# Kernel tuning notes

Hardware: AMD Instinct MI355X
Metric: run time of the kernel (lower is better)

Reference implementation:

```python
import jax, jax.numpy as jnp
import numpy as np

B, N, S, HEADS, D = 8, 512, 64, 16, 256

def setup_inputs() -> dict:
    key = jax.random.key(0)
    ks = jax.random.split(key, 5)
    spatial_pos = jax.random.randint(ks[0], (B, N, S), 0, N)
    H = jax.random.normal(ks[1], (B, N, D), dtype=jnp.float32)
    A = jax.random.uniform(ks[2], (B, N, N), dtype=jnp.float32)
    sigma = jnp.ones((1,), dtype=jnp.float32)
    spatial_emb = jax.random.normal(ks[3], (N, HEADS), dtype=jnp.float32)
    vt_weight = jax.random.normal(ks[4], (1, HEADS), dtype=jnp.float32)
    return {"spatial_pos": spatial_pos, "H": H, "A": A, "sigma": sigma,
            "spatial_emb": spatial_emb, "vt_weight": vt_weight}

def reference(spatial_pos, H, A, sigma, spatial_emb, vt_weight):
    b, n, s = spatial_pos.shape
    heads = spatial_emb.shape[1]
    # padding_idx=0: row 0 of the embedding table is zero
    emb = spatial_emb.at[0].set(0.0)
    spb = emb[spatial_pos]                       # [B, N, S, heads]
    # torch .view reinterprets contiguous memory: reshape, NOT transpose
    spb = spb.reshape(b, heads, n, s)            # [B, heads, N, S]
    spatial_bias = jnp.einsum('bhns,bhms->bhnm', spb, spb)  # [B,heads,N,N]
    # degree-normalized (left) adjacency aggregation
    deg = jnp.sum(A, axis=-1, keepdims=True)     # [B, N, 1]
    nor_A = (deg ** -0.5) * A
    M = jnp.matmul(nor_A, H)                     # [B, N, D]
    # pairwise squared euclidean distance via expansion (same math,
    # avoids materializing [B,N,N,D])
    h2 = jnp.sum(H * H, axis=-1)                 # [B, N]
    m2 = jnp.sum(M * M, axis=-1)                 # [B, N]
    cross = jnp.einsum('bnd,bmd->bnm', H, M)     # [B, N, N]
    d2 = h2[:, :, None] + m2[:, None, :] - 2.0 * cross
    gaussian = jnp.exp(-d2 / (2.0 * sigma[0] ** 2))  # [B, N, N]
    # virtual-token bias (vt_weight) only touches padded row/col 0,
    # which is sliced off before return -> no effect on output.
    return spatial_bias + gaussian[:, None, :, :]  # [B, heads, N, N]
```

## Files before the change

kernel.cpp:

```cpp
#include <hip/hip_runtime.h>
#include <hip/hip_bf16.h>

#define NB 8
#define NN 512
#define NS 64
#define NH 16
#define ND 256

typedef __attribute__((ext_vector_type(8))) short bf16x8;
typedef __attribute__((ext_vector_type(4))) short bf16x4;
typedef __attribute__((ext_vector_type(4))) float f32x4;

__device__ inline float wred(float v) {
#pragma unroll
  for (int m = 32; m; m >>= 1) v += __shfl_xor(v, m, 64);
  return v;
}
__device__ inline float wred16(float v) {
#pragma unroll
  for (int m = 1; m < 16; m <<= 1) v += __shfl_xor(v, m, 64);
  return v;
}
__device__ inline ushort f2bf(float x) {
  __hip_bfloat16 h = __float2bfloat16(x);
  return *(ushort*)&h;
}

__global__ __launch_bounds__(256) void k_prep(const int* __restrict__ pos,
                                              const float* __restrict__ emb,
                                              const float* __restrict__ H,
                                              const float* __restrict__ A,
                                              __hip_bfloat16* __restrict__ spb,
                                              __hip_bfloat16* __restrict__ Ab,
                                              __hip_bfloat16* __restrict__ Hb,
                                              __hip_bfloat16* __restrict__ HT,
                                              float* __restrict__ rdeg,
                                              float* __restrict__ h2) {
  __shared__ ushort T[64][68];
  int blk = blockIdx.x, tid = threadIdx.x;
  int wave = tid >> 6, lane = tid & 63;

  if (blk < 1024) {
    int t = blk * 256 + tid;
    int idx = pos[t];
    __hip_bfloat16* dst = spb + (size_t)t * NH;
    union { bf16x8 v; ushort h[8]; } u0, u1;
    if (idx == 0) {
#pragma unroll
      for (int i = 0; i < 8; ++i) { u0.h[i] = 0; u1.h[i] = 0; }
    } else {
      const float* er = emb + idx * NH;
#pragma unroll
      for (int i = 0; i < 8; ++i) { u0.h[i] = f2bf(er[i]); u1.h[i] = f2bf(er[8 + i]); }
    }
    *(bf16x8*)(void*)dst = u0.v;
    *(bf16x8*)(void*)(dst + 8) = u1.v;
  } else if (blk < 2048) {
    int row = (blk - 1024) * 4 + wave;
    const float* ar = A + (size_t)row * NN;
    float4 v0 = *(const float4*)(ar + lane * 8);
    float4 v1 = *(const float4*)(ar + lane * 8 + 4);
    float s = v0.x + v0.y + v0.z + v0.w + v1.x + v1.y + v1.z + v1.w;
    union { bf16x8 v; ushort h[8]; } u;
    u.h[0] = f2bf(v0.x); u.h[1] = f2bf(v0.y); u.h[2] = f2bf(v0.z); u.h[3] = f2bf(v0.w);
    u.h[4] = f2bf(v1.x); u.h[5] = f2bf(v1.y); u.h[6] = f2bf(v1.z); u.h[7] = f2bf(v1.w);
    *(bf16x8*)(void*)(Ab + (size_t)row * NN + lane * 8) = u.v;
    s = wred(s);
    if (lane == 0) rdeg[row] = rsqrtf(s);
  } else if (blk < 3072) {
    int row = (blk - 2048) * 4 + wave;
    const float* hr = H + (size_t)row * ND;
    float4 v = *(const float4*)(hr + lane * 4);
    float ss = v.x * v.x + v.y * v.y + v.z * v.z + v.w * v.w;
    union { bf16x4 v4; ushort h[4]; } u;
    u.h[0] = f2bf(v.x); u.h[1] = f2bf(v.y); u.h[2] = f2bf(v.z); u.h[3] = f2bf(v.w);
    *(bf16x4*)(void*)(Hb + (size_t)row * ND + lane * 4) = u.v4;
    ss = wred(ss);
    if (lane == 0) h2[row] = ss;
  } else {
    int bi = blk - 3072;
    int b = bi >> 5, r = bi & 31;
    int d0 = (r >> 3) * 64, n0 = (r & 7) * 64;
    int n = tid >> 2, c = (tid & 3) * 16;
    const float* src = H + ((size_t)b * NN + n0 + n) * ND + d0 + c;
#pragma unroll
    for (int q = 0; q < 4; ++q) {
      float4 f = *(const float4*)(src + q * 4);
      T[n][c + q * 4 + 0] = f2bf(f.x);
      T[n][c + q * 4 + 1] = f2bf(f.y);
      T[n][c + q * 4 + 2] = f2bf(f.z);
      T[n][c + q * 4 + 3] = f2bf(f.w);
    }
    __syncthreads();
    int d = tid >> 2, nc = (tid & 3) * 16;
    union { bf16x8 v; ushort h[8]; } o0, o1;
#pragma unroll
    for (int i = 0; i < 8; ++i) { o0.h[i] = T[nc + i][d]; o1.h[i] = T[nc + 8 + i][d]; }
    __hip_bfloat16* dst = HT + ((size_t)b * ND + d0 + d) * NN + n0 + nc;
    *(bf16x8*)(void*)dst = o0.v;
    *(bf16x8*)(void*)(dst + 8) = o1.v;
  }
}

__global__ __launch_bounds__(256) void k_gemmM(const __hip_bfloat16* __restrict__ Ab,
                                               const __hip_bfloat16* __restrict__ HT,
                                               const float* __restrict__ rdeg,
                                               __hip_bfloat16* __restrict__ Mb,
                                               float* __restrict__ m2p) {
  int wave = threadIdx.x >> 6, lane = threadIdx.x & 63;
  int b = blockIdx.x & 7, t = blockIdx.x >> 3;
  int tile = t * 4 + wave;
  int rt = tile >> 3, ct = tile & 7;
  int r0 = rt * 32, c0 = ct * 32;
  int rl = lane & 15, g4 = lane >> 4;
  const __hip_bfloat16* X = Ab + (size_t)b * NN * NN;
  const __hip_bfloat16* Y = HT + (size_t)b * ND * NN;
  f32x4 acc[2][2];
#pragma unroll
  for (int i = 0; i < 2; ++i)
#pragma unroll
    for (int j = 0; j < 2; ++j) { acc[i][j][0] = 0.f; acc[i][j][1] = 0.f; acc[i][j][2] = 0.f; acc[i][j][3] = 0.f; }
#pragma unroll
  for (int kk = 0; kk < NN / 32; ++kk) {
    int kb = kk * 32 + g4 * 8;
    bf16x8 a[2], bv[2];
#pragma unroll
    for (int i = 0; i < 2; ++i)
      a[i] = *(const bf16x8*)(const void*)(X + (size_t)(r0 + i * 16 + rl) * NN + kb);
#pragma unroll
    for (int j = 0; j < 2; ++j)
      bv[j] = *(const bf16x8*)(const void*)(Y + (size_t)(c0 + j * 16 + rl) * NN + kb);
#pragma unroll
    for (int i = 0; i < 2; ++i)
#pragma unroll
      for (int j = 0; j < 2; ++j)
        acc[i][j] = __builtin_amdgcn_mfma_f32_16x16x32_bf16(a[i], bv[j], acc[i][j], 0, 0, 0);
  }
#pragma unroll
  for (int i = 0; i < 2; ++i)
#pragma unroll
    for (int r = 0; r < 4; ++r) {
      int row = r0 + i * 16 + g4 * 4 + r;
      float rd = rdeg[b * NN + row];
      float ss = 0.f;
#pragma unroll
      for (int j = 0; j < 2; ++j) {
        float m = rd * acc[i][j][r];
        int col = c0 + j * 16 + rl;
        Mb[((size_t)b * NN + row) * ND + col] = __float2bfloat16(m);
        ss += m * m;
      }
      ss = wred16(ss);
      if (rl == 0) m2p[(size_t)ct * (NB * NN) + b * NN + row] = ss;
    }
}

__global__ __launch_bounds__(256) void k_out(const __hip_bfloat16* __restrict__ Hb,
                                             const __hip_bfloat16* __restrict__ Mb,
                                             const __hip_bfloat16* __restrict__ spb,
                                             const float* __restrict__ h2,
                                             const float* __restrict__ m2p,
                                             const float* __restrict__ sigma,
                                             float* __restrict__ out) {
  __shared__ float Gt[64][66];
  __shared__ float h2s[64], m2s[64];
  int b = blockIdx.x & 7;
  int t2 = blockIdx.x >> 3;
  int ct = t2 & 7, rt = (t2 >> 3) & 7, hg = t2 >> 6;
  int r0 = rt * 64, c0 = ct * 64;
  int tid = threadIdx.x;
  int wave = tid >> 6, lane = tid & 63;
  int rl = lane & 15, g4 = lane >> 4;

  if (tid < 64) {
    h2s[tid] = h2[b * NN + r0 + tid];
  } else if (tid < 128) {
    int c = tid - 64;
    float s = 0.f;
#pragma unroll
    for (int p = 0; p < 8; ++p) s += m2p[(size_t)p * (NB * NN) + b * NN + c0 + c];
    m2s[c] = s;
  }
  __syncthreads();

  {
    const __hip_bfloat16* X = Hb + (size_t)b * NN * ND;
    const __hip_bfloat16* Y = Mb + (size_t)b * NN * ND;
    int rbase = r0 + wave * 16;
    f32x4 acc[4];
#pragma unroll
    for (int j = 0; j < 4; ++j) { acc[j][0] = 0.f; acc[j][1] = 0.f; acc[j][2] = 0.f; acc[j][3] = 0.f; }
#pragma unroll
    for (int kk = 0; kk < ND / 32; ++kk) {
      int kb = kk * 32 + g4 * 8;
      bf16x8 a = *(const bf16x8*)(const void*)(X + (size_t)(rbase + rl) * ND + kb);
#pragma unroll
      for (int j = 0; j < 4; ++j) {
        bf16x8 bv = *(const bf16x8*)(const void*)(Y + (size_t)(c0 + j * 16 + rl) * ND + kb);
        acc[j] = __builtin_amdgcn_mfma_f32_16x16x32_bf16(a, bv, acc[j], 0, 0, 0);
      }
    }
    float sg = sigma[0];
    float inv = 0.5f / (sg * sg);
#pragma unroll
    for (int j = 0; j < 4; ++j)
#pragma unroll
      for (int r = 0; r < 4; ++r) {
        int rowl = wave * 16 + g4 * 4 + r;
        int col = j * 16 + rl;
        float d2 = h2s[rowl] + m2s[col] - 2.0f * acc[j][r];
        Gt[rowl][col] = __expf(-d2 * inv);
      }
  }
  __syncthreads();

#pragma unroll
  for (int hh = 0; hh < 2; ++hh) {
    int h = hg * 8 + wave * 2 + hh;
    const __hip_bfloat16* X = spb + ((size_t)b * NH + h) * NN * NS;
    f32x4 acc[4][4];
#pragma unroll
    for (int i = 0; i < 4; ++i)
#pragma unroll
      for (int j = 0; j < 4; ++j) { acc[i][j][0] = 0.f; acc[i][j][1] = 0.f; acc[i][j][2] = 0.f; acc[i][j][3] = 0.f; }
#pragma unroll
    for (int kk = 0; kk < NS / 32; ++kk) {
      int kb = kk * 32 + g4 * 8;
      bf16x8 a[4], bv[4];
#pragma unroll
      for (int i = 0; i < 4; ++i)
        a[i] = *(const bf16x8*)(const void*)(X + (size_t)(r0 + i * 16 + rl) * NS + kb);
#pragma unroll
      for (int j = 0; j < 4; ++j)
        bv[j] = *(const bf16x8*)(const void*)(X + (size_t)(c0 + j * 16 + rl) * NS + kb);
#pragma unroll
      for (int i = 0; i < 4; ++i)
#pragma unroll
        for (int j = 0; j < 4; ++j)
          acc[i][j] = __builtin_amdgcn_mfma_f32_16x16x32_bf16(a[i], bv[j], acc[i][j], 0, 0, 0);
    }
    float* ob = out + ((size_t)b * NH + h) * NN * NN;
#pragma unroll
    for (int i = 0; i < 4; ++i)
#pragma unroll
      for (int j = 0; j < 4; ++j)
#pragma unroll
        for (int r = 0; r < 4; ++r) {
          int rowl = i * 16 + g4 * 4 + r;
          int col = j * 16 + rl;
          ob[(size_t)(r0 + rowl) * NN + c0 + col] = acc[i][j][r] + Gt[rowl][col];
        }
  }
}

extern "C" void kernel_launch(void* const* d_in, const int* in_sizes, int n_in,
                              void* d_out, int out_size, void* d_ws, size_t ws_size,
                              hipStream_t stream) {
  const int* pos = (const int*)d_in[0];
  const float* H = (const float*)d_in[1];
  const float* A = (const float*)d_in[2];
  const float* sigma = (const float*)d_in[3];
  const float* emb = (const float*)d_in[4];
  float* out = (float*)d_out;

  char* ws = (char*)d_ws;
  size_t off = 0;
  auto alloc = [&](size_t bytes) -> void* {
    void* p = ws + off;
    off = (off + bytes + 255) & ~(size_t)255;
    return p;
  };
  __hip_bfloat16* spb = (__hip_bfloat16*)alloc((size_t)NB * NH * NN * NS * 2);
  __hip_bfloat16* Ab  = (__hip_bfloat16*)alloc((size_t)NB * NN * NN * 2);
  __hip_bfloat16* Hb  = (__hip_bfloat16*)alloc((size_t)NB * NN * ND * 2);
  __hip_bfloat16* HT  = (__hip_bfloat16*)alloc((size_t)NB * ND * NN * 2);
  __hip_bfloat16* Mb  = (__hip_bfloat16*)alloc((size_t)NB * NN * ND * 2);
  float* m2p  = (float*)alloc((size_t)8 * NB * NN * 4);
  float* rdeg = (float*)alloc((size_t)NB * NN * 4);
  float* h2   = (float*)alloc((size_t)NB * NN * 4);

  k_prep<<<3328, 256, 0, stream>>>(pos, emb, H, A, spb, Ab, Hb, HT, rdeg, h2);
  k_gemmM<<<256, 256, 0, stream>>>(Ab, HT, rdeg, Mb, m2p);
  k_out<<<1024, 256, 0, stream>>>(Hb, Mb, spb, h2, m2p, sigma, out);
}
```

Before: 76.05 us.

## Stage output tiles through LDS for float4 stores, loop all heads per block

```diff
diff --git a/kernel.cpp b/kernel.cpp
--- a/kernel.cpp
+++ b/kernel.cpp
@@ -111,62 +111,53 @@
   int b = blockIdx.x & 7, t = blockIdx.x >> 3;
   int tile = t * 4 + wave;
   int rt = tile >> 3, ct = tile & 7;
-  int r0 = rt * 32, c0 = ct * 32;
+  int r0 = rt * 16, c0 = ct * 32;
   int rl = lane & 15, g4 = lane >> 4;
   const __hip_bfloat16* X = Ab + (size_t)b * NN * NN;
   const __hip_bfloat16* Y = HT + (size_t)b * ND * NN;
-  f32x4 acc[2][2];
-#pragma unroll
-  for (int i = 0; i < 2; ++i)
-#pragma unroll
-    for (int j = 0; j < 2; ++j) { acc[i][j][0] = 0.f; acc[i][j][1] = 0.f; acc[i][j][2] = 0.f; acc[i][j][3] = 0.f; }
+  f32x4 acc[2];
+#pragma unroll
+  for (int j = 0; j < 2; ++j) { acc[j][0] = 0.f; acc[j][1] = 0.f; acc[j][2] = 0.f; acc[j][3] = 0.f; }
 #pragma unroll
   for (int kk = 0; kk < NN / 32; ++kk) {
     int kb = kk * 32 + g4 * 8;
-    bf16x8 a[2], bv[2];
-#pragma unroll
-    for (int i = 0; i < 2; ++i)
-      a[i] = *(const bf16x8*)(const void*)(X + (size_t)(r0 + i * 16 + rl) * NN + kb);
-#pragma unroll
-    for (int j = 0; j < 2; ++j)
-      bv[j] = *(const bf16x8*)(const void*)(Y + (size_t)(c0 + j * 16 + rl) * NN + kb);
-#pragma unroll
-    for (int i = 0; i < 2; ++i)
-#pragma unroll
-      for (int j = 0; j < 2; ++j)
-        acc[i][j] = __builtin_amdgcn_mfma_f32_16x16x32_bf16(a[i], bv[j], acc[i][j], 0, 0, 0);
-  }
-#pragma unroll
-  for (int i = 0; i < 2; ++i)
-#pragma unroll
-    for (int r = 0; r < 4; ++r) {
-      int row = r0 + i * 16 + g4 * 4 + r;
-      float rd = rdeg[b * NN + row];
-      float ss = 0.f;
-#pragma unroll
-      for (int j = 0; j < 2; ++j) {
-        float m = rd * acc[i][j][r];
-        int col = c0 + j * 16 + rl;
-        Mb[((size_t)b * NN + row) * ND + col] = __float2bfloat16(m);
-        ss += m * m;
-      }
-      ss = wred16(ss);
-      if (rl == 0) m2p[(size_t)ct * (NB * NN) + b * NN + row] = ss;
-    }
-}
-
-__global__ __launch_bounds__(256) void k_out(const __hip_bfloat16* __restrict__ Hb,
+    bf16x8 a = *(const bf16x8*)(const void*)(X + (size_t)(r0 + rl) * NN + kb);
+#pragma unroll
+    for (int j = 0; j < 2; ++j) {
+      bf16x8 bv = *(const bf16x8*)(const void*)(Y + (size_t)(c0 + j * 16 + rl) * NN + kb);
+      acc[j] = __builtin_amdgcn_mfma_f32_16x16x32_bf16(a, bv, acc[j], 0, 0, 0);
+    }
+  }
+#pragma unroll
+  for (int r = 0; r < 4; ++r) {
+    int row = r0 + g4 * 4 + r;
+    float rd = rdeg[b * NN + row];
+    float ss = 0.f;
+#pragma unroll
+    for (int j = 0; j < 2; ++j) {
+      float m = rd * acc[j][r];
+      int col = c0 + j * 16 + rl;
+      Mb[((size_t)b * NN + row) * ND + col] = __float2bfloat16(m);
+      ss += m * m;
+    }
+    ss = wred16(ss);
+    if (rl == 0) m2p[(size_t)ct * (NB * NN) + b * NN + row] = ss;
+  }
+}
+
+__global__ __launch_bounds__(512) void k_out(const __hip_bfloat16* __restrict__ Hb,
                                              const __hip_bfloat16* __restrict__ Mb,
                                              const __hip_bfloat16* __restrict__ spb,
                                              const float* __restrict__ h2,
                                              const float* __restrict__ m2p,
                                              const float* __restrict__ sigma,
                                              float* __restrict__ out) {
-  __shared__ float Gt[64][66];
+  __shared__ __align__(16) float Gt[64][68];
+  __shared__ __align__(16) float Ot[2][64][68];
   __shared__ float h2s[64], m2s[64];
   int b = blockIdx.x & 7;
   int t2 = blockIdx.x >> 3;
-  int ct = t2 & 7, rt = (t2 >> 3) & 7, hg = t2 >> 6;
+  int ct = t2 & 7, rt = t2 >> 3;
   int r0 = rt * 64, c0 = ct * 64;
   int tid = threadIdx.x;
   int wave = tid >> 6, lane = tid & 63;
@@ -186,70 +177,72 @@
   {
     const __hip_bfloat16* X = Hb + (size_t)b * NN * ND;
     const __hip_bfloat16* Y = Mb + (size_t)b * NN * ND;
-    int rbase = r0 + wave * 16;
-    f32x4 acc[4];
-#pragma unroll
-    for (int j = 0; j < 4; ++j) { acc[j][0] = 0.f; acc[j][1] = 0.f; acc[j][2] = 0.f; acc[j][3] = 0.f; }
+    int rw = (wave & 3) * 16, cw = (wave >> 2) * 32;
+    f32x4 acc[2];
+#pragma unroll
+    for (int j = 0; j < 2; ++j) { acc[j][0] = 0.f; acc[j][1] = 0.f; acc[j][2] = 0.f; acc[j][3] = 0.f; }
 #pragma unroll
     for (int kk = 0; kk < ND / 32; ++kk) {
       int kb = kk * 32 + g4 * 8;
-      bf16x8 a = *(const bf16x8*)(const void*)(X + (size_t)(rbase + rl) * ND + kb);
-#pragma unroll
-      for (int j = 0; j < 4; ++j) {
-        bf16x8 bv = *(const bf16x8*)(const void*)(Y + (size_t)(c0 + j * 16 + rl) * ND + kb);
+      bf16x8 a = *(const bf16x8*)(const void*)(X + (size_t)(r0 + rw + rl) * ND + kb);
+#pragma unroll
+      for (int j = 0; j < 2; ++j) {
+        bf16x8 bv = *(const bf16x8*)(const void*)(Y + (size_t)(c0 + cw + j * 16 + rl) * ND + kb);
         acc[j] = __builtin_amdgcn_mfma_f32_16x16x32_bf16(a, bv, acc[j], 0, 0, 0);
       }
     }
     float sg = sigma[0];
     float inv = 0.5f / (sg * sg);
 #pragma unroll
-    for (int j = 0; j < 4; ++j)
+    for (int j = 0; j < 2; ++j)
 #pragma unroll
       for (int r = 0; r < 4; ++r) {
-        int rowl = wave * 16 + g4 * 4 + r;
-        int col = j * 16 + rl;
+        int rowl = rw + g4 * 4 + r;
+        int col = cw + j * 16 + rl;
         float d2 = h2s[rowl] + m2s[col] - 2.0f * acc[j][r];
         Gt[rowl][col] = __expf(-d2 * inv);
       }
   }
   __syncthreads();
 
-#pragma unroll
-  for (int hh = 0; hh < 2; ++hh) {
-    int h = hg * 8 + wave * 2 + hh;
-    const __hip_bfloat16* X = spb + ((size_t)b * NH + h) * NN * NS;
-    f32x4 acc[4][4];
-#pragma unroll
-    for (int i = 0; i < 4; ++i)
-#pragma unroll
-      for (int j = 0; j < 4; ++j) { acc[i][j][0] = 0.f; acc[i][j][1] = 0.f; acc[i][j][2] = 0.f; acc[i][j][3] = 0.f; }
+  int grp = wave >> 2, wg = wave & 3;
+  int tl = tid & 255;
+#pragma unroll 1
+  for (int hp = 0; hp < 8; ++hp) {
+    int h = hp * 2 + grp;
+    const __hip_bfloat16* Xs = spb + ((size_t)b * NH + h) * NN * NS;
+    int rw = wg * 16;
+    f32x4 acc[4];
+#pragma unroll
+    for (int j = 0; j < 4; ++j) { acc[j][0] = 0.f; acc[j][1] = 0.f; acc[j][2] = 0.f; acc[j][3] = 0.f; }
 #pragma unroll
     for (int kk = 0; kk < NS / 32; ++kk) {
       int kb = kk * 32 + g4 * 8;
-      bf16x8 a[4], bv[4];
-#pragma unroll
-      for (int i = 0; i < 4; ++i)
-        a[i] = *(const bf16x8*)(const void*)(X + (size_t)(r0 + i * 16 + rl) * NS + kb);
-#pragma unroll
-      for (int j = 0; j < 4; ++j)
-        bv[j] = *(const bf16x8*)(const void*)(X + (size_t)(c0 + j * 16 + rl) * NS + kb);
-#pragma unroll
-      for (int i = 0; i < 4; ++i)
-#pragma unroll
-        for (int j = 0; j < 4; ++j)
-          acc[i][j] = __builtin_amdgcn_mfma_f32_16x16x32_bf16(a[i], bv[j], acc[i][j], 0, 0, 0);
-    }
+      bf16x8 a = *(const bf16x8*)(const void*)(Xs + (size_t)(r0 + rw + rl) * NS + kb);
+#pragma unroll
+      for (int j = 0; j < 4; ++j) {
+        bf16x8 bv = *(const bf16x8*)(const void*)(Xs + (size_t)(c0 + j * 16 + rl) * NS + kb);
+        acc[j] = __builtin_amdgcn_mfma_f32_16x16x32_bf16(a, bv, acc[j], 0, 0, 0);
+      }
+    }
+#pragma unroll
+    for (int j = 0; j < 4; ++j)
+#pragma unroll
+      for (int r = 0; r < 4; ++r)
+        Ot[grp][rw + g4 * 4 + r][j * 16 + rl] = acc[j][r];
+    __syncthreads();
     float* ob = out + ((size_t)b * NH + h) * NN * NN;
-#pragma unroll
-    for (int i = 0; i < 4; ++i)
-#pragma unroll
-      for (int j = 0; j < 4; ++j)
-#pragma unroll
-        for (int r = 0; r < 4; ++r) {
-          int rowl = i * 16 + g4 * 4 + r;
-          int col = j * 16 + rl;
-          ob[(size_t)(r0 + rowl) * NN + c0 + col] = acc[i][j][r] + Gt[rowl][col];
-        }
+    int srow = tl >> 4, scol = (tl & 15) * 4;
+#pragma unroll
+    for (int it = 0; it < 4; ++it) {
+      int row = srow + it * 16;
+      float4 g = *(const float4*)&Gt[row][scol];
+      float4 o = *(const float4*)&Ot[grp][row][scol];
+      float4 w;
+      w.x = g.x + o.x; w.y = g.y + o.y; w.z = g.z + o.z; w.w = g.w + o.w;
+      *(float4*)&ob[(size_t)(r0 + row) * NN + c0 + scol] = w;
+    }
+    __syncthreads();
   }
 }
 
@@ -280,6 +273,6 @@
   float* h2   = (float*)alloc((size_t)NB * NN * 4);
 
   k_prep<<<3328, 256, 0, stream>>>(pos, emb, H, A, spb, Ab, Hb, HT, rdeg, h2);
-  k_gemmM<<<256, 256, 0, stream>>>(Ab, HT, rdeg, Mb, m2p);
-  k_out<<<1024, 256, 0, stream>>>(Hb, Mb, spb, h2, m2p, sigma, out);
-}
+  k_gemmM<<<512, 256, 0, stream>>>(Ab, HT, rdeg, Mb, m2p);
+  k_out<<<512, 512, 0, stream>>>(Hb, Mb, spb, h2, m2p, sigma, out);
+}
```

Result: slower. 85.96 us (+13.0%).

## Process all heads per block and stage output through LDS for float4 stores

Applied to the files above, without the earlier changes.

```diff
diff --git a/kernel.cpp b/kernel.cpp
--- a/kernel.cpp
+++ b/kernel.cpp
@@ -162,11 +162,12 @@
                                              const float* __restrict__ m2p,
                                              const float* __restrict__ sigma,
                                              float* __restrict__ out) {
-  __shared__ float Gt[64][66];
+  __shared__ __align__(16) float Gt[64][68];
+  __shared__ __align__(16) float Ot[4][16][68];
   __shared__ float h2s[64], m2s[64];
   int b = blockIdx.x & 7;
   int t2 = blockIdx.x >> 3;
-  int ct = t2 & 7, rt = (t2 >> 3) & 7, hg = t2 >> 6;
+  int ct = t2 & 7, rt = t2 >> 3;
   int r0 = rt * 64, c0 = ct * 64;
   int tid = threadIdx.x;
   int wave = tid >> 6, lane = tid & 63;
@@ -186,14 +187,14 @@
   {
     const __hip_bfloat16* X = Hb + (size_t)b * NN * ND;
     const __hip_bfloat16* Y = Mb + (size_t)b * NN * ND;
-    int rbase = r0 + wave * 16;
+    int rw = wave * 16;
     f32x4 acc[4];
 #pragma unroll
     for (int j = 0; j < 4; ++j) { acc[j][0] = 0.f; acc[j][1] = 0.f; acc[j][2] = 0.f; acc[j][3] = 0.f; }
 #pragma unroll
     for (int kk = 0; kk < ND / 32; ++kk) {
       int kb = kk * 32 + g4 * 8;
-      bf16x8 a = *(const bf16x8*)(const void*)(X + (size_t)(rbase + rl) * ND + kb);
+      bf16x8 a = *(const bf16x8*)(const void*)(X + (size_t)(r0 + rw + rl) * ND + kb);
 #pragma unroll
       for (int j = 0; j < 4; ++j) {
         bf16x8 bv = *(const bf16x8*)(const void*)(Y + (size_t)(c0 + j * 16 + rl) * ND + kb);
@@ -206,7 +207,7 @@
     for (int j = 0; j < 4; ++j)
 #pragma unroll
       for (int r = 0; r < 4; ++r) {
-        int rowl = wave * 16 + g4 * 4 + r;
+        int rowl = rw + g4 * 4 + r;
         int col = j * 16 + rl;
         float d2 = h2s[rowl] + m2s[col] - 2.0f * acc[j][r];
         Gt[rowl][col] = __expf(-d2 * inv);
@@ -214,10 +215,11 @@
   }
   __syncthreads();
 
-#pragma unroll
-  for (int hh = 0; hh < 2; ++hh) {
-    int h = hg * 8 + wave * 2 + hh;
-    const __hip_bfloat16* X = spb + ((size_t)b * NH + h) * NN * NS;
+  float (*Ow)[68] = Ot[wave];
+#pragma unroll 1
+  for (int hh = 0; hh < 4; ++hh) {
+    int h = wave * 4 + hh;
+    const __hip_bfloat16* Xs = spb + ((size_t)b * NH + h) * NN * NS;
     f32x4 acc[4][4];
 #pragma unroll
     for (int i = 0; i < 4; ++i)
@@ -229,10 +231,10 @@
       bf16x8 a[4], bv[4];
 #pragma unroll
       for (int i = 0; i < 4; ++i)
-        a[i] = *(const bf16x8*)(const void*)(X + (size_t)(r0 + i * 16 + rl) * NS + kb);
+        a[i] = *(const bf16x8*)(const void*)(Xs + (size_t)(r0 + i * 16 + rl) * NS + kb);
 #pragma unroll
       for (int j = 0; j < 4; ++j)
-        bv[j] = *(const bf16x8*)(const void*)(X + (size_t)(c0 + j * 16 + rl) * NS + kb);
+        bv[j] = *(const bf16x8*)(const void*)(Xs + (size_t)(c0 + j * 16 + rl) * NS + kb);
 #pragma unroll
       for (int i = 0; i < 4; ++i)
 #pragma unroll
@@ -240,16 +242,26 @@
           acc[i][j] = __builtin_amdgcn_mfma_f32_16x16x32_bf16(a[i], bv[j], acc[i][j], 0, 0, 0);
     }
     float* ob = out + ((size_t)b * NH + h) * NN * NN;
-#pragma unroll
-    for (int i = 0; i < 4; ++i)
+#pragma unroll 1
+    for (int i = 0; i < 4; ++i) {
 #pragma unroll
       for (int j = 0; j < 4; ++j)
 #pragma unroll
-        for (int r = 0; r < 4; ++r) {
-          int rowl = i * 16 + g4 * 4 + r;
-          int col = j * 16 + rl;
-          ob[(size_t)(r0 + rowl) * NN + c0 + col] = acc[i][j][r] + Gt[rowl][col];
-        }
+        for (int r = 0; r < 4; ++r)
+          Ow[g4 * 4 + r][j * 16 + rl] = acc[i][j][r];
+      asm volatile("s_waitcnt lgkmcnt(0)" ::: "memory");
+#pragma unroll
+      for (int it = 0; it < 4; ++it) {
+        int row = it * 4 + (lane >> 4);
+        int col = (lane & 15) * 4;
+        float4 o = *(const float4*)&Ow[row][col];
+        float4 g = *(const float4*)&Gt[i * 16 + row][col];
+        float4 w;
+        w.x = g.x + o.x; w.y = g.y + o.y; w.z = g.z + o.z; w.w = g.w + o.w;
+        *(float4*)&ob[(size_t)(r0 + i * 16 + row) * NN + c0 + col] = w;
+      }
+      asm volatile("" ::: "memory");
+    }
   }
 }
 
@@ -281,5 +293,5 @@
 
   k_prep<<<3328, 256, 0, stream>>>(pos, emb, H, A, spb, Ab, Hb, HT, rdeg, h2);
   k_gemmM<<<256, 256, 0, stream>>>(Ab, HT, rdeg, Mb, m2p);
-  k_out<<<1024, 256, 0, stream>>>(Hb, Mb, spb, h2, m2p, sigma, out);
-}
+  k_out<<<512, 256, 0, stream>>>(Hb, Mb, spb, h2, m2p, sigma, out);
+}
```

Result: slower. 97.07 us (+27.6%).

## Split gaussian into separate kernel and swizzle prep block order

Applied to the files above, without the earlier changes.

```diff
diff --git a/kernel.cpp b/kernel.cpp
--- a/kernel.cpp
+++ b/kernel.cpp
@@ -41,7 +41,9 @@
   int wave = tid >> 6, lane = tid & 63;
 
   if (blk < 1024) {
-    int t = blk * 256 + tid;
+    int q = blk;
+    int qs = (q & 7) * 128 + (q >> 3);
+    int t = qs * 256 + tid;
     int idx = pos[t];
     __hip_bfloat16* dst = spb + (size_t)t * NH;
     union { bf16x8 v; ushort h[8]; } u0, u1;
@@ -56,7 +58,9 @@
     *(bf16x8*)(void*)dst = u0.v;
     *(bf16x8*)(void*)(dst + 8) = u1.v;
   } else if (blk < 2048) {
-    int row = (blk - 1024) * 4 + wave;
+    int q = blk - 1024;
+    int qs = (q & 7) * 128 + (q >> 3);
+    int row = qs * 4 + wave;
     const float* ar = A + (size_t)row * NN;
     float4 v0 = *(const float4*)(ar + lane * 8);
     float4 v1 = *(const float4*)(ar + lane * 8 + 4);
@@ -68,7 +72,9 @@
     s = wred(s);
     if (lane == 0) rdeg[row] = rsqrtf(s);
   } else if (blk < 3072) {
-    int row = (blk - 2048) * 4 + wave;
+    int q = blk - 2048;
+    int qs = (q & 7) * 128 + (q >> 3);
+    int row = qs * 4 + wave;
     const float* hr = H + (size_t)row * ND;
     float4 v = *(const float4*)(hr + lane * 4);
     float ss = v.x * v.x + v.y * v.y + v.z * v.z + v.w * v.w;
@@ -79,7 +85,8 @@
     if (lane == 0) h2[row] = ss;
   } else {
     int bi = blk - 3072;
-    int b = bi >> 5, r = bi & 31;
+    int bis = (bi & 7) * 32 + (bi >> 3);
+    int b = bis >> 5, r = bis & 31;
     int d0 = (r >> 3) * 64, n0 = (r & 7) * 64;
     int n = tid >> 2, c = (tid & 3) * 16;
     const float* src = H + ((size_t)b * NN + n0 + n) * ND + d0 + c;
@@ -155,18 +162,16 @@
     }
 }
 
-__global__ __launch_bounds__(256) void k_out(const __hip_bfloat16* __restrict__ Hb,
-                                             const __hip_bfloat16* __restrict__ Mb,
-                                             const __hip_bfloat16* __restrict__ spb,
-                                             const float* __restrict__ h2,
-                                             const float* __restrict__ m2p,
-                                             const float* __restrict__ sigma,
-                                             float* __restrict__ out) {
-  __shared__ float Gt[64][66];
+__global__ __launch_bounds__(256) void k_gauss(const __hip_bfloat16* __restrict__ Hb,
+                                               const __hip_bfloat16* __restrict__ Mb,
+                                               const float* __restrict__ h2,
+                                               const float* __restrict__ m2p,
+                                               const float* __restrict__ sigma,
+                                               float* __restrict__ G) {
   __shared__ float h2s[64], m2s[64];
   int b = blockIdx.x & 7;
   int t2 = blockIdx.x >> 3;
-  int ct = t2 & 7, rt = (t2 >> 3) & 7, hg = t2 >> 6;
+  int ct = t2 & 7, rt = t2 >> 3;
   int r0 = rt * 64, c0 = ct * 64;
   int tid = threadIdx.x;
   int wave = tid >> 6, lane = tid & 63;
@@ -183,74 +188,81 @@
   }
   __syncthreads();
 
-  {
-    const __hip_bfloat16* X = Hb + (size_t)b * NN * ND;
-    const __hip_bfloat16* Y = Mb + (size_t)b * NN * ND;
-    int rbase = r0 + wave * 16;
-    f32x4 acc[4];
-#pragma unroll
-    for (int j = 0; j < 4; ++j) { acc[j][0] = 0.f; acc[j][1] = 0.f; acc[j][2] = 0.f; acc[j][3] = 0.f; }
-#pragma unroll
-    for (int kk = 0; kk < ND / 32; ++kk) {
-      int kb = kk * 32 + g4 * 8;
-      bf16x8 a = *(const bf16x8*)(const void*)(X + (size_t)(rbase + rl) * ND + kb);
-#pragma unroll
-      for (int j = 0; j < 4; ++j) {
-        bf16x8 bv = *(const bf16x8*)(const void*)(Y + (size_t)(c0 + j * 16 + rl) * ND + kb);
-        acc[j] = __builtin_amdgcn_mfma_f32_16x16x32_bf16(a, bv, acc[j], 0, 0, 0);
+  const __hip_bfloat16* X = Hb + (size_t)b * NN * ND;
+  const __hip_bfloat16* Y = Mb + (size_t)b * NN * ND;
+  int rw = wave * 16;
+  f32x4 acc[4];
+#pragma unroll
+  for (int j = 0; j < 4; ++j) { acc[j][0] = 0.f; acc[j][1] = 0.f; acc[j][2] = 0.f; acc[j][3] = 0.f; }
+#pragma unroll
+  for (int kk = 0; kk < ND / 32; ++kk) {
+    int kb = kk * 32 + g4 * 8;
+    bf16x8 a = *(const bf16x8*)(const void*)(X + (size_t)(r0 + rw + rl) * ND + kb);
+#pragma unroll
+    for (int j = 0; j < 4; ++j) {
+      bf16x8 bv = *(const bf16x8*)(const void*)(Y + (size_t)(c0 + j * 16 + rl) * ND + kb);
+      acc[j] = __builtin_amdgcn_mfma_f32_16x16x32_bf16(a, bv, acc[j], 0, 0, 0);
+    }
+  }
+  float sg = sigma[0];
+  float inv = 0.5f / (sg * sg);
+  float* Gb = G + (size_t)b * NN * NN;
+#pragma unroll
+  for (int j = 0; j < 4; ++j)
+#pragma unroll
+    for (int r = 0; r < 4; ++r) {
+      int row = r0 + rw + g4 * 4 + r;
+      int col = c0 + j * 16 + rl;
+      float d2 = h2s[rw + g4 * 4 + r] + m2s[j * 16 + rl] - 2.0f * acc[j][r];
+      Gb[(size_t)row * NN + col] = __expf(-d2 * inv);
+    }
+}
+
+__global__ __launch_bounds__(256) void k_out(const __hip_bfloat16* __restrict__ spb,
+                                             const float* __restrict__ G,
+                                             float* __restrict__ out) {
+  int b = blockIdx.x & 7;
+  int t2 = blockIdx.x >> 3;
+  int ct = t2 & 7, rt = (t2 >> 3) & 7, hg = t2 >> 6;
+  int r0 = rt * 64, c0 = ct * 64;
+  int wave = threadIdx.x >> 6, lane = threadIdx.x & 63;
+  int rl = lane & 15, g4 = lane >> 4;
+  int h = hg * 4 + wave;
+
+  const __hip_bfloat16* Xs = spb + ((size_t)b * NH + h) * NN * NS;
+  f32x4 acc[4][4];
+#pragma unroll
+  for (int i = 0; i < 4; ++i)
+#pragma unroll
+    for (int j = 0; j < 4; ++j) { acc[i][j][0] = 0.f; acc[i][j][1] = 0.f; acc[i][j][2] = 0.f; acc[i][j][3] = 0.f; }
+#pragma unroll
+  for (int kk = 0; kk < NS / 32; ++kk) {
+    int kb = kk * 32 + g4 * 8;
+    bf16x8 a[4], bv[4];
+#pragma unroll
+    for (int i = 0; i < 4; ++i)
+      a[i] = *(const bf16x8*)(const void*)(Xs + (size_t)(r0 + i * 16 + rl) * NS + kb);
+#pragma unroll
+    for (int j = 0; j < 4; ++j)
+      bv[j] = *(const bf16x8*)(const void*)(Xs + (size_t)(c0 + j * 16 + rl) * NS + kb);
+#pragma unroll
+    for (int i = 0; i < 4; ++i)
+#pragma unroll
+      for (int j = 0; j < 4; ++j)
+        acc[i][j] = __builtin_amdgcn_mfma_f32_16x16x32_bf16(a[i], bv[j], acc[i][j], 0, 0, 0);
+  }
+  const float* Gb = G + (size_t)b * NN * NN;
+  float* ob = out + ((size_t)b * NH + h) * NN * NN;
+#pragma unroll
+  for (int i = 0; i < 4; ++i)
+#pragma unroll
+    for (int j = 0; j < 4; ++j)
+#pragma unroll
+      for (int r = 0; r < 4; ++r) {
+        int row = r0 + i * 16 + g4 * 4 + r;
+        int col = c0 + j * 16 + rl;
+        ob[(size_t)row * NN + col] = acc[i][j][r] + Gb[(size_t)row * NN + col];
       }
-    }
-    float sg = sigma[0];
-    float inv = 0.5f / (sg * sg);
-#pragma unroll
-    for (int j = 0; j < 4; ++j)
-#pragma unroll
-      for (int r = 0; r < 4; ++r) {
-        int rowl = wave * 16 + g4 * 4 + r;
-        int col = j * 16 + rl;
-        float d2 = h2s[rowl] + m2s[col] - 2.0f * acc[j][r];
-        Gt[rowl][col] = __expf(-d2 * inv);
-      }
-  }
-  __syncthreads();
-
-#pragma unroll
-  for (int hh = 0; hh < 2; ++hh) {
-    int h = hg * 8 + wave * 2 + hh;
-    const __hip_bfloat16* X = spb + ((size_t)b * NH + h) * NN * NS;
-    f32x4 acc[4][4];
-#pragma unroll
-    for (int i = 0; i < 4; ++i)
-#pragma unroll
-      for (int j = 0; j < 4; ++j) { acc[i][j][0] = 0.f; acc[i][j][1] = 0.f; acc[i][j][2] = 0.f; acc[i][j][3] = 0.f; }
-#pragma unroll
-    for (int kk = 0; kk < NS / 32; ++kk) {
-      int kb = kk * 32 + g4 * 8;
-      bf16x8 a[4], bv[4];
-#pragma unroll
-      for (int i = 0; i < 4; ++i)
-        a[i] = *(const bf16x8*)(const void*)(X + (size_t)(r0 + i * 16 + rl) * NS + kb);
-#pragma unroll
-      for (int j = 0; j < 4; ++j)
-        bv[j] = *(const bf16x8*)(const void*)(X + (size_t)(c0 + j * 16 + rl) * NS + kb);
-#pragma unroll
-      for (int i = 0; i < 4; ++i)
-#pragma unroll
-        for (int j = 0; j < 4; ++j)
-          acc[i][j] = __builtin_amdgcn_mfma_f32_16x16x32_bf16(a[i], bv[j], acc[i][j], 0, 0, 0);
-    }
-    float* ob = out + ((size_t)b * NH + h) * NN * NN;
-#pragma unroll
-    for (int i = 0; i < 4; ++i)
-#pragma unroll
-      for (int j = 0; j < 4; ++j)
-#pragma unroll
-        for (int r = 0; r < 4; ++r) {
-          int rowl = i * 16 + g4 * 4 + r;
-          int col = j * 16 + rl;
-          ob[(size_t)(r0 + rowl) * NN + c0 + col] = acc[i][j][r] + Gt[rowl][col];
-        }
-  }
 }
 
 extern "C" void kernel_launch(void* const* d_in, const int* in_sizes, int n_in,
@@ -275,11 +287,13 @@
   __hip_bfloat16* Hb  = (__hip_bfloat16*)alloc((size_t)NB * NN * ND * 2);
   __hip_bfloat16* HT  = (__hip_bfloat16*)alloc((size_t)NB * ND * NN * 2);
   __hip_bfloat16* Mb  = (__hip_bfloat16*)alloc((size_t)NB * NN * ND * 2);
+  float* Gws  = (float*)alloc((size_t)NB * NN * NN * 4);
   float* m2p  = (float*)alloc((size_t)8 * NB * NN * 4);
   float* rdeg = (float*)alloc((size_t)NB * NN * 4);
   float* h2   = (float*)alloc((size_t)NB * NN * 4);
 
   k_prep<<<3328, 256, 0, stream>>>(pos, emb, H, A, spb, Ab, Hb, HT, rdeg, h2);
   k_gemmM<<<256, 256, 0, stream>>>(Ab, HT, rdeg, Mb, m2p);
-  k_out<<<1024, 256, 0, stream>>>(Hb, Mb, spb, h2, m2p, sigma, out);
-}
+  k_gauss<<<512, 256, 0, stream>>>(Hb, Mb, h2, m2p, sigma, Gws);
+  k_out<<<2048, 256, 0, stream>>>(spb, Gws, out);
+}
```

After: 101.0 us. 1.33x slower.
